# Performance work log

Hardware: AMD Instinct MI355X
Metric: run time of the kernel (lower is better)

The kernel has to match this reference:

```python
import jax, jax.numpy as jnp
import numpy as np

TOPK = 2
ALPHA = 32.0
EPS = 1e-20


def setup_inputs() -> dict:
    key = jax.random.key(0)
    ks = jax.random.split(key, 6)
    E, D, R, Q, V = 16, 2048, 16, 2048, 512
    B, S = 2, 2048
    return {
        "hidden_states": jax.random.normal(ks[0], (B, S, D), jnp.float32),
        "router_weight": jax.random.normal(ks[1], (E, D), jnp.float32) * 0.02,
        "q_lora_a": jax.random.normal(ks[2], (E, D, R), jnp.float32) * 0.02,
        "q_lora_b": jax.random.normal(ks[3], (E, R, Q), jnp.float32) * 0.02,
        "v_lora_a": jax.random.normal(ks[4], (E, D, R), jnp.float32) * 0.02,
        "v_lora_b": jax.random.normal(ks[5], (E, R, V), jnp.float32) * 0.02,
    }


def reference(hidden_states, router_weight, q_lora_a, q_lora_b, v_lora_a, v_lora_b):
    E, D, R = q_lora_a.shape
    Qo = q_lora_b.shape[-1]
    Vo = v_lora_b.shape[-1]
    scale = ALPHA / float(R)
    orig_shape = hidden_states.shape[:-1]
    h = hidden_states.reshape(-1, D)  # [n, D]
    n = h.shape[0]

    # router: top-k softmax probs, renormalized over the k selected experts
    logits = jnp.einsum('nd,ed->ne', h, router_weight)
    probs = jax.nn.softmax(logits, axis=-1)
    scores, idx = jax.lax.top_k(probs, TOPK)          # [n, k]
    scores = scores / (scores.sum(-1, keepdims=True) + EPS)

    # per-token expert combine weights c[n, e] = scale * sum_k score_k * 1[idx_k == e]
    c = jnp.zeros((n, E), h.dtype).at[jnp.arange(n)[:, None], idx].add(scores * scale)

    # dense per-expert low-rank projections; weighting by c makes non-selected
    # experts contribute zero -> identical math to gather + einsum + weighted sum.
    q_low = jnp.einsum('nd,edr->ner', h, q_lora_a) * c[..., None]  # [n, E, R]
    v_low = jnp.einsum('nd,edr->ner', h, v_lora_a) * c[..., None]
    q_delta = jnp.einsum('ner,erq->nq', q_low, q_lora_b)
    v_delta = jnp.einsum('ner,erv->nv', v_low, v_lora_b)

    return (q_delta.reshape(*orig_shape, Qo), v_delta.reshape(*orig_shape, Vo))
```

## Files before the change

kernel.cpp:

```cpp
#include <hip/hip_runtime.h>
#include <math.h>

#define DD 2048
#define EE 16
#define RR 16
#define QO 2048
#define VO 512
#define DSPLIT 4
#define DRANGE (DD / DSPLIT)
#define DC 64
#define RDC 256
#define DSPL 8
#define TB 32
#define ABLK 8
#define T2 32
#define CGQ (QO / 256)
#define CGV (VO / 256)

struct Route { int i0, i1; float w0, w1; };

__global__ __launch_bounds__(256) void logits_kernel(
    const float* __restrict__ h, const float* __restrict__ rw,
    double* __restrict__ lgp, int* __restrict__ cnt, int n)
{
    __shared__ float hs[8 * RDC];

    if (blockIdx.x == 0 && blockIdx.y == 0 && threadIdx.x < EE)
        cnt[threadIdx.x] = 0;

    int t0 = blockIdx.x * 8;
    int ds = blockIdx.y;
    int d0 = ds * RDC;
    int e  = threadIdx.x >> 4;
    int l  = threadIdx.x & 15;

    for (int i = threadIdx.x; i < 8 * (RDC / 4); i += 256) {
        int t = i >> 6, dq = (i & 63) * 4;
        float4 v = make_float4(0.f, 0.f, 0.f, 0.f);
        if (t0 + t < n)
            v = *(const float4*)&h[(size_t)(t0 + t) * DD + d0 + dq];
        *(float4*)&hs[t * RDC + dq] = v;
    }
    __syncthreads();

    double acc[8];
#pragma unroll
    for (int t = 0; t < 8; ++t) acc[t] = 0.0;

    const float* rwe = rw + e * DD + d0;
#pragma unroll
    for (int g = 0; g < RDC / 64; ++g) {
        int d = g * 64 + l * 4;
        float4 r4 = *(const float4*)&rwe[d];
        double rx = r4.x, ry = r4.y, rz = r4.z, rw4 = r4.w;
#pragma unroll
        for (int t = 0; t < 8; ++t) {
            float4 hv = *(const float4*)&hs[t * RDC + d];
            acc[t] += (double)hv.x * rx + (double)hv.y * ry
                    + (double)hv.z * rz + (double)hv.w * rw4;
        }
    }
#pragma unroll
    for (int t = 0; t < 8; ++t) {
#pragma unroll
        for (int off = 8; off; off >>= 1)
            acc[t] += __shfl_down(acc[t], off, 16);
    }
    if (l == 0) {
#pragma unroll
        for (int t = 0; t < 8; ++t) {
            int tok = t0 + t;
            if (tok < n)
                lgp[((size_t)tok * DSPL + ds) * EE + e] = acc[t];
        }
    }
}

__global__ __launch_bounds__(256) void finalize_kernel(
    const double* __restrict__ lgp, Route* __restrict__ route,
    unsigned short* __restrict__ bucket, int* __restrict__ cnt, int n)
{
    int j   = threadIdx.x >> 4;
    int l   = threadIdx.x & 15;
    int tok = blockIdx.x * 16 + j;
    if (tok >= n) return;

    const double* p = lgp + (size_t)tok * (DSPL * EE) + l;
    double s = 0.0;
#pragma unroll
    for (int ds = 0; ds < DSPL; ++ds) s += p[ds * EE];

    double m1 = s; int i1 = l;
#pragma unroll
    for (int off = 8; off; off >>= 1) {
        double om = __shfl_xor(m1, off, 16);
        int    oi = __shfl_xor(i1, off, 16);
        if (om > m1 || (om == m1 && oi < i1)) { m1 = om; i1 = oi; }
    }
    double s2 = (l == i1) ? -1.0e300 : s;
    double m2 = s2; int i2 = l;
#pragma unroll
    for (int off = 8; off; off >>= 1) {
        double om = __shfl_xor(m2, off, 16);
        int    oi = __shfl_xor(i2, off, 16);
        if (om > m2 || (om == m2 && oi < i2)) { m2 = om; i2 = oi; }
    }
    if (l == 0) {
        double ed = exp(m2 - m1);
        double w0 = 2.0 / (1.0 + ed);
        Route rt;
        rt.i0 = i1; rt.i1 = i2;
        rt.w0 = (float)w0;
        rt.w1 = (float)(2.0 - w0);
        route[tok] = rt;
        int p0 = atomicAdd(&cnt[i1], 1);
        bucket[(size_t)i1 * n + p0] = (unsigned short)(tok * 2);
        int p1 = atomicAdd(&cnt[i2], 1);
        bucket[(size_t)i2 * n + p1] = (unsigned short)(tok * 2 + 1);
    }
}

__device__ __forceinline__ void loadh(float (&hv)[4][8],
        const float* const (&hp)[8], int d0) {
#pragma unroll
    for (int dd = 0; dd < 4; ++dd)
#pragma unroll
        for (int ti = 0; ti < 8; ++ti)
            hv[dd][ti] = hp[ti][d0 + dd * 16];
}

__device__ __forceinline__ void computeh(float (&accq)[8][4], float (&accv)[8][4],
        const float (&hv)[4][8], const float* aq, const float* av,
        int d0, int s, int rp) {
#pragma unroll
    for (int dd = 0; dd < 4; ++dd) {
        int d = d0 + dd * 16 + s;
        float4 aqv = *(const float4*)&aq[d * RR + rp * 4];
        float4 avv = *(const float4*)&av[d * RR + rp * 4];
        const float* ap = &aqv.x;
        const float* vp = &avv.x;
#pragma unroll
        for (int ti = 0; ti < 8; ++ti) {
            float hvv = hv[dd][ti];
#pragma unroll
            for (int ri = 0; ri < 4; ++ri) {
                accq[ti][ri] = fmaf(hvv, ap[ri], accq[ti][ri]);
                accv[ti][ri] = fmaf(hvv, vp[ri], accv[ti][ri]);
            }
        }
    }
}

__global__ __launch_bounds__(256, 2) void a_kernel(
    const float* __restrict__ h, const Route* __restrict__ route,
    const unsigned short* __restrict__ bucket, const int* __restrict__ cnt,
    const float* __restrict__ qa, const float* __restrict__ va,
    float* __restrict__ low, int n)
{
    int e  = blockIdx.x;
    int ds = blockIdx.z;
    int cnt_e = cnt[e];
    if ((int)(blockIdx.y * TB) >= cnt_e) return;

    __align__(16) __shared__ float aq_s[DRANGE * RR];
    __align__(16) __shared__ float av_s[DRANGE * RR];

    const int dbase = ds * DRANGE;
    const float* qa_e = qa + ((size_t)e * DD + dbase) * RR;
    const float* va_e = va + ((size_t)e * DD + dbase) * RR;

#pragma unroll
    for (int k = 0; k < 8; ++k) {
        int t = (k << 8) + threadIdx.x;
        *(float4*)&aq_s[t * 4] = *(const float4*)&qa_e[(size_t)t * 4];
        *(float4*)&av_s[t * 4] = *(const float4*)&va_e[(size_t)t * 4];
    }
    __syncthreads();

    int lane = threadIdx.x & 63;
    int w    = threadIdx.x >> 6;
    int s    = lane & 15;
    int rp   = lane >> 4;

    for (int cb = blockIdx.y * TB; cb < cnt_e; cb += gridDim.y * TB) {
        int cw = cb + w * 8;
        if (cw >= cnt_e) continue;

        int sl = 0; float wt = 0.f;
        int idx = cw + lane;
        if (lane < 8 && idx < cnt_e) {
            sl = bucket[(size_t)e * n + idx];
            Route rt = route[sl >> 1];
            wt = (sl & 1) ? rt.w1 : rt.w0;
        }
        const float* hp[8];
        int   slots[8];
        float wts[8];
#pragma unroll
        for (int ti = 0; ti < 8; ++ti) {
            slots[ti] = __shfl(sl, ti);
            wts[ti]   = __shfl(wt, ti);
            hp[ti]    = h + (size_t)(slots[ti] >> 1) * DD + dbase + s;
        }

        float accq[8][4], accv[8][4];
#pragma unroll
        for (int ti = 0; ti < 8; ++ti)
#pragma unroll
            for (int ri = 0; ri < 4; ++ri) { accq[ti][ri] = 0.f; accv[ti][ri] = 0.f; }

        float hvA[4][8], hvB[4][8];
        loadh(hvA, hp, 0);
#pragma unroll
        for (int d0 = 0; d0 < DRANGE; d0 += 2 * DC) {
            loadh(hvB, hp, d0 + DC);
            computeh(accq, accv, hvA, aq_s, av_s, d0, s, rp);
            if (d0 + 2 * DC < DRANGE) loadh(hvA, hp, d0 + 2 * DC);
            computeh(accq, accv, hvB, aq_s, av_s, d0 + DC, s, rp);
        }

#pragma unroll
        for (int ti = 0; ti < 8; ++ti)
#pragma unroll
            for (int ri = 0; ri < 4; ++ri) {
#pragma unroll
                for (int off = 8; off; off >>= 1) {
                    accq[ti][ri] += __shfl_down(accq[ti][ri], off, 16);
                    accv[ti][ri] += __shfl_down(accv[ti][ri], off, 16);
                }
            }
        if (s == 0) {
#pragma unroll
            for (int ti = 0; ti < 8; ++ti) {
                if (cw + ti < cnt_e) {
                    int   sl2 = slots[ti];
                    float wt2 = wts[ti];
                    size_t base = ((size_t)sl2 * DSPLIT + ds) * 32;
                    float4 q4 = make_float4(accq[ti][0] * wt2, accq[ti][1] * wt2,
                                            accq[ti][2] * wt2, accq[ti][3] * wt2);
                    float4 v4 = make_float4(accv[ti][0] * wt2, accv[ti][1] * wt2,
                                            accv[ti][2] * wt2, accv[ti][3] * wt2);
                    *(float4*)&low[base + rp * 4]      = q4;
                    *(float4*)&low[base + 16 + rp * 4] = v4;
                }
            }
        }
    }
}

__global__ __launch_bounds__(256) void b_kernel(
    const Route* __restrict__ route, const float* __restrict__ low,
    const float* __restrict__ qb, const float* __restrict__ vb,
    float* __restrict__ outq, float* __restrict__ outv, int n)
{
    int t0 = blockIdx.x * T2;
    int cg = blockIdx.y;
    int tid = threadIdx.x;

    __shared__ float acc_s[T2 * 256];
    __shared__ float ls[T2 * 2 * RR];
    __shared__ int   elist[EE * T2];
    __shared__ int   ecnt[EE];
    __shared__ Route rts[T2];

    if (tid < EE) ecnt[tid] = 0;
    if (tid < T2) {
        int tok = t0 + tid;
        if (tok < n) rts[tid] = route[tok];
        else { rts[tid].i0 = -1; rts[tid].i1 = -1; rts[tid].w0 = 0.f; rts[tid].w1 = 0.f; }
    }
    __syncthreads();
    if (tid < T2 * 2) {
        int j = tid >> 1, k = tid & 1;
        int e = k ? rts[j].i1 : rts[j].i0;
        if (e >= 0) {
            int p = atomicAdd(&ecnt[e], 1);
            elist[e * T2 + p] = j * 2 + k;
        }
    }
    int side = (cg >= CGQ) ? 1 : 0;
    {
        int slot = tid >> 2, r4 = (tid & 3) * 4;
        int j = slot >> 1, k = slot & 1;
        int tok = t0 + j;
        float4 v = make_float4(0.f, 0.f, 0.f, 0.f);
        if (tok < n) {
            const float* lp = low + (size_t)(tok * 2 + k) * (DSPLIT * 32) + side * 16 + r4;
            float4 p0 = *(const float4*)(lp);
            float4 p1 = *(const float4*)(lp + 32);
            float4 p2 = *(const float4*)(lp + 64);
            float4 p3 = *(const float4*)(lp + 96);
            v.x = p0.x + p1.x + p2.x + p3.x;
            v.y = p0.y + p1.y + p2.y + p3.y;
            v.z = p0.z + p1.z + p2.z + p3.z;
            v.w = p0.w + p1.w + p2.w + p3.w;
        }
        *(float4*)&ls[slot * RR + r4] = v;
    }
#pragma unroll
    for (int j = 0; j < T2; ++j) acc_s[j * 256 + tid] = 0.f;
    __syncthreads();

    const float* bp; float* outp; int W, colbase;
    if (cg < CGQ) { bp = qb; outp = outq; W = QO; colbase = cg * 256; }
    else          { bp = vb; outp = outv; W = VO; colbase = (cg - CGQ) * 256; }
    int col = colbase + tid;

    float bcA[RR], bcB[RR];
    {
        const float* be = bp + col;
#pragma unroll
        for (int r = 0; r < RR; ++r) bcA[r] = be[(size_t)r * W];
    }

#define PROC_E(EI, BC)                                                      \
    {                                                                       \
        int c = ecnt[EI];                                                   \
        for (int ii = 0; ii < c; ++ii) {                                    \
            int sk = elist[(EI) * T2 + ii];                                 \
            const float* lp = &ls[sk * RR];                                 \
            float4 l0 = *(const float4*)(lp);                               \
            float4 l1 = *(const float4*)(lp + 4);                           \
            float4 l2 = *(const float4*)(lp + 8);                           \
            float4 l3 = *(const float4*)(lp + 12);                          \
            float v = 0.f;                                                  \
            v = fmaf(l0.x, BC[0],  v); v = fmaf(l0.y, BC[1],  v);           \
            v = fmaf(l0.z, BC[2],  v); v = fmaf(l0.w, BC[3],  v);           \
            v = fmaf(l1.x, BC[4],  v); v = fmaf(l1.y, BC[5],  v);           \
            v = fmaf(l1.z, BC[6],  v); v = fmaf(l1.w, BC[7],  v);           \
            v = fmaf(l2.x, BC[8],  v); v = fmaf(l2.y, BC[9],  v);           \
            v = fmaf(l2.z, BC[10], v); v = fmaf(l2.w, BC[11], v);           \
            v = fmaf(l3.x, BC[12], v); v = fmaf(l3.y, BC[13], v);           \
            v = fmaf(l3.z, BC[14], v); v = fmaf(l3.w, BC[15], v);           \
            acc_s[(sk >> 1) * 256 + tid] += v;   \
        }                                                                   \
    }

    for (int e = 0; e < EE; e += 2) {
        {
            const float* bn = bp + (size_t)(e + 1) * RR * W + col;
#pragma unroll
            for (int r = 0; r < RR; ++r) bcB[r] = bn[(size_t)r * W];
        }
        PROC_E(e, bcA);
        if (e + 2 < EE) {
            const float* bn = bp + (size_t)(e + 2) * RR * W + col;
#pragma unroll
            for (int r = 0; r < RR; ++r) bcA[r] = bn[(size_t)r * W];
        }
        PROC_E(e + 1, bcB);
    }
#undef PROC_E

#pragma unroll
    for (int j = 0; j < T2; ++j) {
        int tok = t0 + j;
        if (tok < n) outp[(size_t)tok * W + col] = acc_s[j * 256 + tid];
    }
}

extern "C" void kernel_launch(void* const* d_in, const int* in_sizes, int n_in,
                              void* d_out, int out_size, void* d_ws, size_t ws_size,
                              hipStream_t stream) {
    const float* h  = (const float*)d_in[0];
    const float* rw = (const float*)d_in[1];
    const float* qa = (const float*)d_in[2];
    const float* qb = (const float*)d_in[3];
    const float* va = (const float*)d_in[4];
    const float* vb = (const float*)d_in[5];

    int n = in_sizes[0] / DD;
    float* out  = (float*)d_out;
    float* outq = out;
    float* outv = out + (size_t)n * QO;

    char* ws = (char*)d_ws;
    Route* route = (Route*)ws;
    size_t off = ((size_t)n * sizeof(Route) + 255) & ~(size_t)255;
    int* cnt = (int*)(ws + off);
    off = (off + EE * sizeof(int) + 255) & ~(size_t)255;
    unsigned short* bucket = (unsigned short*)(ws + off);
    off = (off + (size_t)EE * n * sizeof(unsigned short) + 255) & ~(size_t)255;
    float* low = (float*)(ws + off);
    double* lgp = (double*)low;

    dim3 g1((n + 7) / 8, DSPL);
    logits_kernel<<<g1, 256, 0, stream>>>(h, rw, lgp, cnt, n);

    finalize_kernel<<<(n + 15) / 16, 256, 0, stream>>>(lgp, route, bucket, cnt, n);

    dim3 g2(EE, ABLK, DSPLIT);
    a_kernel<<<g2, 256, 0, stream>>>(h, route, bucket, cnt, qa, va, low, n);

    dim3 g3((n + T2 - 1) / T2, CGQ + CGV);
    b_kernel<<<g3, 256, 0, stream>>>(route, low, qb, vb, outq, outv, n);
}
```

Before: 236.7 us.

## Pad expert LoRA-A smem rows and halve tokens per wave in a_kernel

Cuts the tokens each wave processes in the expert A-projection from 8 to 4 and the tokens per block from 32 to 16, and sets ABLK from 8 to 16, which likely doubles the y-grid of blocks. The LoRA-A tiles in shared memory now use a padded row stride of 20 floats instead of 16 to reduce LDS bank conflicts on the float4 reads. The aim is more parallelism and lower register pressure, at the cost of more shared memory per block (about 80 KB, which may limit occupancy) and less reuse of each A tile per wave.

Result: faster. 214.3 us (-9.5%).

```diff
diff --git a/kernel.cpp b/kernel.cpp
--- a/kernel.cpp
+++ b/kernel.cpp
@@ -9,10 +9,12 @@
 #define DSPLIT 4
 #define DRANGE (DD / DSPLIT)
 #define DC 64
+#define ASTR 20
 #define RDC 256
 #define DSPL 8
-#define TB 32
-#define ABLK 8
+#define TW 4
+#define TBI (TW * 4)
+#define ABLK 16
 #define T2 32
 #define CGQ (QO / 256)
 #define CGV (VO / 256)
@@ -120,27 +122,27 @@
     }
 }
 
-__device__ __forceinline__ void loadh(float (&hv)[4][8],
-        const float* const (&hp)[8], int d0) {
+__device__ __forceinline__ void loadh(float (&hv)[4][TW],
+        const float* const (&hp)[TW], int d0) {
 #pragma unroll
     for (int dd = 0; dd < 4; ++dd)
 #pragma unroll
-        for (int ti = 0; ti < 8; ++ti)
+        for (int ti = 0; ti < TW; ++ti)
             hv[dd][ti] = hp[ti][d0 + dd * 16];
 }
 
-__device__ __forceinline__ void computeh(float (&accq)[8][4], float (&accv)[8][4],
-        const float (&hv)[4][8], const float* aq, const float* av,
+__device__ __forceinline__ void computeh(float (&accq)[TW][4], float (&accv)[TW][4],
+        const float (&hv)[4][TW], const float* aq, const float* av,
         int d0, int s, int rp) {
 #pragma unroll
     for (int dd = 0; dd < 4; ++dd) {
         int d = d0 + dd * 16 + s;
-        float4 aqv = *(const float4*)&aq[d * RR + rp * 4];
-        float4 avv = *(const float4*)&av[d * RR + rp * 4];
+        float4 aqv = *(const float4*)&aq[d * ASTR + rp * 4];
+        float4 avv = *(const float4*)&av[d * ASTR + rp * 4];
         const float* ap = &aqv.x;
         const float* vp = &avv.x;
 #pragma unroll
-        for (int ti = 0; ti < 8; ++ti) {
+        for (int ti = 0; ti < TW; ++ti) {
             float hvv = hv[dd][ti];
 #pragma unroll
             for (int ri = 0; ri < 4; ++ri) {
@@ -160,20 +162,19 @@
     int e  = blockIdx.x;
     int ds = blockIdx.z;
     int cnt_e = cnt[e];
-    if ((int)(blockIdx.y * TB) >= cnt_e) return;
-
-    __align__(16) __shared__ float aq_s[DRANGE * RR];
-    __align__(16) __shared__ float av_s[DRANGE * RR];
+    if ((int)(blockIdx.y * TBI) >= cnt_e) return;
+
+    __align__(16) __shared__ float aq_s[DRANGE * ASTR];
+    __align__(16) __shared__ float av_s[DRANGE * ASTR];
 
     const int dbase = ds * DRANGE;
     const float* qa_e = qa + ((size_t)e * DD + dbase) * RR;
     const float* va_e = va + ((size_t)e * DD + dbase) * RR;
 
-#pragma unroll
-    for (int k = 0; k < 8; ++k) {
-        int t = (k << 8) + threadIdx.x;
-        *(float4*)&aq_s[t * 4] = *(const float4*)&qa_e[(size_t)t * 4];
-        *(float4*)&av_s[t * 4] = *(const float4*)&va_e[(size_t)t * 4];
+    for (int i = threadIdx.x; i < DRANGE * RR / 4; i += 256) {
+        int d = i >> 2, rf = (i & 3) * 4;
+        *(float4*)&aq_s[d * ASTR + rf] = *(const float4*)&qa_e[(size_t)i * 4];
+        *(float4*)&av_s[d * ASTR + rf] = *(const float4*)&va_e[(size_t)i * 4];
     }
     __syncthreads();
 
@@ -182,34 +183,33 @@
     int s    = lane & 15;
     int rp   = lane >> 4;
 
-    for (int cb = blockIdx.y * TB; cb < cnt_e; cb += gridDim.y * TB) {
-        int cw = cb + w * 8;
+    for (int cb = blockIdx.y * TBI; cb < cnt_e; cb += gridDim.y * TBI) {
+        int cw = cb + w * TW;
         if (cw >= cnt_e) continue;
 
         int sl = 0; float wt = 0.f;
-        int idx = cw + lane;
-        if (lane < 8 && idx < cnt_e) {
-            sl = bucket[(size_t)e * n + idx];
+        if (lane < TW && cw + lane < cnt_e) {
+            sl = bucket[(size_t)e * n + cw + lane];
             Route rt = route[sl >> 1];
             wt = (sl & 1) ? rt.w1 : rt.w0;
         }
-        const float* hp[8];
-        int   slots[8];
-        float wts[8];
-#pragma unroll
-        for (int ti = 0; ti < 8; ++ti) {
+        const float* hp[TW];
+        int   slots[TW];
+        float wts[TW];
+#pragma unroll
+        for (int ti = 0; ti < TW; ++ti) {
             slots[ti] = __shfl(sl, ti);
             wts[ti]   = __shfl(wt, ti);
             hp[ti]    = h + (size_t)(slots[ti] >> 1) * DD + dbase + s;
         }
 
-        float accq[8][4], accv[8][4];
-#pragma unroll
-        for (int ti = 0; ti < 8; ++ti)
+        float accq[TW][4], accv[TW][4];
+#pragma unroll
+        for (int ti = 0; ti < TW; ++ti)
 #pragma unroll
             for (int ri = 0; ri < 4; ++ri) { accq[ti][ri] = 0.f; accv[ti][ri] = 0.f; }
 
-        float hvA[4][8], hvB[4][8];
+        float hvA[4][TW], hvB[4][TW];
         loadh(hvA, hp, 0);
 #pragma unroll
         for (int d0 = 0; d0 < DRANGE; d0 += 2 * DC) {
@@ -220,7 +220,7 @@
         }
 
 #pragma unroll
-        for (int ti = 0; ti < 8; ++ti)
+        for (int ti = 0; ti < TW; ++ti)
 #pragma unroll
             for (int ri = 0; ri < 4; ++ri) {
 #pragma unroll
@@ -231,7 +231,7 @@
             }
         if (s == 0) {
 #pragma unroll
-            for (int ti = 0; ti < 8; ++ti) {
+            for (int ti = 0; ti < TW; ++ti) {
                 if (cw + ti < cnt_e) {
                     int   sl2 = slots[ti];
                     float wt2 = wts[ti];
```
